# Kernel tuning notes

Measured on AMD Instinct MI355X. Metric: run time of the kernel, lower is better.

Reference implementation:

```python
import jax, jax.numpy as jnp
import numpy as np
import math

QUERY_DIM = 128
SCALE = 1.0 / math.sqrt(QUERY_DIM)

def setup_inputs() -> dict:
    key = jax.random.key(0)
    k1, k2, k3 = jax.random.split(key, 3)
    B, Q, K, D = 16, 2048, 2048, 128
    return {
        "query": jax.random.normal(k1, (B, Q, D), dtype=jnp.float32),
        "keys": jax.random.normal(k2, (B, K, D), dtype=jnp.float32),
        "values": jax.random.normal(k3, (B, K, D), dtype=jnp.float32),
    }

def reference(query, keys, values):
    # energy[b,q,k] = sum_d query[b,q,d] * keys[b,k,d], scaled then softmax over k
    energy = jnp.einsum("bqd,bkd->bqk", query, keys) * SCALE
    attn = jax.nn.softmax(energy, axis=2)
    # linear combination over values
    return jnp.einsum("bqk,bkv->bqv", attn, values)
```

## Files before the change

### kernel.cpp

```cpp
#include <hip/hip_runtime.h>
#include <hip/hip_bf16.h>


#define BATCH 16
#define QLEN 2048
#define KLEN 2048
#define DIM 128
#define BM 64
#define BN 64
#define NT (KLEN / BN)

#define KBYTES 16384
#define BUFBYTES 32768

typedef __attribute__((ext_vector_type(8))) short bf16x8;
typedef __attribute__((ext_vector_type(4))) float f32x4;

__device__ __forceinline__ short f2bf(float x) {
    union { float f; unsigned u; } v; v.f = x;
    unsigned r = v.u + 0x7FFFu + ((v.u >> 16) & 1u);
    return (short)(r >> 16);
}
__device__ __forceinline__ unsigned pkbf(float a, float b) {
    __hip_bfloat162 h = __float22bfloat162_rn(float2{a, b});
    union { __hip_bfloat162 h; unsigned u; } c; c.h = h;
    return c.u;
}

#define GLOAD_LDS16(g, l) \
    __builtin_amdgcn_global_load_lds((__attribute__((address_space(1))) void*)(g), \
                                     (__attribute__((address_space(3))) void*)(l), 16, 0, 0)

#define TSTR 72
__global__ __launch_bounds__(256) void prepass_kernel(
    const float* __restrict__ kg, const float* __restrict__ vg,
    unsigned short* __restrict__ Kws, unsigned short* __restrict__ Vtws)
{
    __shared__ unsigned short T[DIM * TSTR];
    const int tid = threadIdx.x;
    const int kb  = blockIdx.x * BN;
    const int b   = blockIdx.y;
    const float* kt = kg + ((size_t)b * KLEN + kb) * DIM;
    const float* vt = vg + ((size_t)b * KLEN + kb) * DIM;
    unsigned short* ko = Kws + ((size_t)b * KLEN + kb) * DIM;
#pragma unroll
    for (int j = 0; j < 8; ++j) {
        int idx = tid + 256 * j;
        int key = idx >> 5;
        int d4  = (idx & 31) * 4;
        float4 kv = *(const float4*)(kt + key * DIM + d4);
        uint2 w; w.x = pkbf(kv.x, kv.y); w.y = pkbf(kv.z, kv.w);
        *(uint2*)(ko + key * DIM + d4) = w;
        float4 vv = *(const float4*)(vt + key * DIM + d4);
        T[(d4 + 0) * TSTR + key] = (unsigned short)f2bf(vv.x);
        T[(d4 + 1) * TSTR + key] = (unsigned short)f2bf(vv.y);
        T[(d4 + 2) * TSTR + key] = (unsigned short)f2bf(vv.z);
        T[(d4 + 3) * TSTR + key] = (unsigned short)f2bf(vv.w);
    }
    __syncthreads();
    unsigned short* vo = Vtws + (size_t)b * DIM * KLEN + kb;
#pragma unroll
    for (int j = 0; j < 4; ++j) {
        int c = tid + 256 * j;
        int d = c >> 3;
        int g = c & 7;
        uint4 u = *(const uint4*)&T[d * TSTR + g * 8];
        *(uint4*)(vo + (size_t)d * KLEN + g * 8) = u;
    }
}

__global__ __launch_bounds__(256, 2) void attn_flash_kernel(
    const float* __restrict__ qg,
    const unsigned short* __restrict__ Kws,
    const unsigned short* __restrict__ Vtws,
    float* __restrict__ outg)
{
    __shared__ __align__(16) char SMC[2 * BUFBYTES];

    const int tid  = threadIdx.x;
    const int wave = tid >> 6;
    const int lane = tid & 63;
    const int lm   = lane & 15;
    const int quad = lane >> 4;
    const int rw   = wave >> 1;
    const int kw   = wave & 1;
    const int b     = blockIdx.y;
    const int qbase = blockIdx.x * BM + rw * 32;

    const float QSCALE = 0.08838834764831845f * 1.4426950408889634f;

    bf16x8 qfA[4], qfB[4];
    {
        const float* qrowA = qg + (size_t)(b * QLEN + qbase + lm) * DIM;
        const float* qrowB = qrowA + 16 * DIM;
#pragma unroll
        for (int dk = 0; dk < 4; ++dk) {
            int d0 = dk * 32 + quad * 8;
            float4 a = *(const float4*)(qrowA + d0);
            float4 c = *(const float4*)(qrowA + d0 + 4);
            uint4 u;
            u.x = pkbf(a.x*QSCALE, a.y*QSCALE); u.y = pkbf(a.z*QSCALE, a.w*QSCALE);
            u.z = pkbf(c.x*QSCALE, c.y*QSCALE); u.w = pkbf(c.z*QSCALE, c.w*QSCALE);
            qfA[dk] = *(bf16x8*)&u;
            float4 e = *(const float4*)(qrowB + d0);
            float4 g = *(const float4*)(qrowB + d0 + 4);
            uint4 v;
            v.x = pkbf(e.x*QSCALE, e.y*QSCALE); v.y = pkbf(e.z*QSCALE, e.w*QSCALE);
            v.z = pkbf(g.x*QSCALE, g.y*QSCALE); v.w = pkbf(g.z*QSCALE, g.w*QSCALE);
            qfB[dk] = *(bf16x8*)&v;
        }
    }

    f32x4 OA[8], OB[8];
#pragma unroll
    for (int i = 0; i < 8; ++i) { OA[i] = 0.0f; OB[i] = 0.0f; }
    float lrA = 0.f, lrB = 0.f;

    const unsigned short* Kb  = Kws  + (size_t)b * KLEN * DIM;
    const unsigned short* Vtb = Vtws + (size_t)b * DIM * KLEN;
    const char* kdma[4];
    const char* vdma[4];
    {
        int gk = lane & 15;
        int r0 = wave * 16 + (lane >> 4);
        int gv = lane & 7;
        int d0v = wave * 32 + (lane >> 3);
#pragma unroll
        for (int i = 0; i < 4; ++i) {
            int r = r0 + 4 * i;
            int key = (r & 3) | ((r & 4) << 1) | ((r & 8) << 1) | ((r & 16) >> 2) | (r & 32);
            kdma[i] = (const char*)Kb + key * 256 + ((gk ^ (r & 15)) << 4);
            int dv = d0v + 8 * i;
            vdma[i] = (const char*)Vtb + (size_t)dv * (KLEN * 2) + ((gv ^ (dv & 7)) << 4);
        }
    }

    int kfo[4];
#pragma unroll
    for (int dk = 0; dk < 4; ++dk)
        kfo[dk] = (kw * 32 + lm) * 256 + (((dk * 4 + quad) ^ lm) << 4);
    const int vfo = lm * 128 + (((kw * 4 + quad) ^ (lm & 7)) << 4);

    auto dma = [&](int tt, int bb) {
        char* ldsK = SMC + bb * BUFBYTES + wave * 4096;
        char* ldsV = ldsK + KBYTES;
        size_t ko = (size_t)tt * 16384;
        size_t vo = (size_t)tt * 128;
#pragma unroll
        for (int i = 0; i < 4; ++i) {
            GLOAD_LDS16(kdma[i] + ko, ldsK + i * 1024);
            GLOAD_LDS16(vdma[i] + vo, ldsV + i * 1024);
        }
    };

    dma(0, 0);
    __syncthreads();

    for (int t = 0; t < NT; ++t) {
        if (t + 1 < NT) dma(t + 1, (t + 1) & 1);

        const char* bufK = SMC + (t & 1) * BUFBYTES;
        const char* bufV = bufK + KBYTES;

        f32x4 S0a = 0.0f, S1a = 0.0f, S0b = 0.0f, S1b = 0.0f;
#pragma unroll
        for (int dk = 0; dk < 4; ++dk) {
            bf16x8 kf0 = *(const bf16x8*)(bufK + kfo[dk]);
            bf16x8 kf1 = *(const bf16x8*)(bufK + kfo[dk] + 4096);
            S0a = __builtin_amdgcn_mfma_f32_16x16x32_bf16(kf0, qfA[dk], S0a, 0, 0, 0);
            S0b = __builtin_amdgcn_mfma_f32_16x16x32_bf16(kf0, qfB[dk], S0b, 0, 0, 0);
            S1a = __builtin_amdgcn_mfma_f32_16x16x32_bf16(kf1, qfA[dk], S1a, 0, 0, 0);
            S1b = __builtin_amdgcn_mfma_f32_16x16x32_bf16(kf1, qfB[dk], S1b, 0, 0, 0);
        }

        float a0 = exp2f(S0a[0]), a1 = exp2f(S0a[1]), a2 = exp2f(S0a[2]), a3 = exp2f(S0a[3]);
        float a4 = exp2f(S1a[0]), a5 = exp2f(S1a[1]), a6 = exp2f(S1a[2]), a7 = exp2f(S1a[3]);
        float b0 = exp2f(S0b[0]), b1 = exp2f(S0b[1]), b2 = exp2f(S0b[2]), b3 = exp2f(S0b[3]);
        float b4 = exp2f(S1b[0]), b5 = exp2f(S1b[1]), b6 = exp2f(S1b[2]), b7 = exp2f(S1b[3]);
        uint4 puA, puB;
        puA.x = pkbf(a0,a1); puA.y = pkbf(a2,a3); puA.z = pkbf(a4,a5); puA.w = pkbf(a6,a7);
        puB.x = pkbf(b0,b1); puB.y = pkbf(b2,b3); puB.z = pkbf(b4,b5); puB.w = pkbf(b6,b7);
        bf16x8 pfA = *(bf16x8*)&puA;
        bf16x8 pfB = *(bf16x8*)&puB;
        lrA += ((a0+a1)+(a2+a3)) + ((a4+a5)+(a6+a7));
        lrB += ((b0+b1)+(b2+b3)) + ((b4+b5)+(b6+b7));

#pragma unroll
        for (int dt = 0; dt < 8; ++dt) {
            bf16x8 vf = *(const bf16x8*)(bufV + vfo + dt * 2048);
            OA[dt] = __builtin_amdgcn_mfma_f32_16x16x32_bf16(vf, pfA, OA[dt], 0, 0, 0);
            OB[dt] = __builtin_amdgcn_mfma_f32_16x16x32_bf16(vf, pfB, OB[dt], 0, 0, 0);
        }

        __syncthreads();
    }

    lrA += __shfl_xor(lrA, 16, 64); lrA += __shfl_xor(lrA, 32, 64);
    lrB += __shfl_xor(lrB, 16, 64); lrB += __shfl_xor(lrB, 32, 64);

    float* Orw = (float*)SMC + rw * 4288;
    if (kw == 1) {
#pragma unroll
        for (int dt = 0; dt < 8; ++dt) {
            *(f32x4*)&Orw[lm*132        + dt*16 + quad*4] = OA[dt];
            *(f32x4*)&Orw[(16+lm)*132   + dt*16 + quad*4] = OB[dt];
        }
        if (lane < 16)      Orw[4224 + lm]      = lrA;
        else if (lane < 32) Orw[4224 + 16 + lm] = lrB;
    }
    __syncthreads();
    if (kw == 0) {
        float invA = 1.0f / (lrA + Orw[4224 + lm]);
        float invB = 1.0f / (lrB + Orw[4224 + 16 + lm]);
        float* orowA = outg + (size_t)(b * QLEN + qbase + lm) * DIM;
        float* orowB = orowA + 16 * DIM;
#pragma unroll
        for (int dt = 0; dt < 8; ++dt) {
            f32x4 oA = *(const f32x4*)&Orw[lm*132      + dt*16 + quad*4];
            f32x4 oB = *(const f32x4*)&Orw[(16+lm)*132 + dt*16 + quad*4];
            *(f32x4*)&orowA[dt*16 + quad*4] = (OA[dt] + oA) * invA;
            *(f32x4*)&orowB[dt*16 + quad*4] = (OB[dt] + oB) * invB;
        }
    }
}

extern "C" void kernel_launch(void* const* d_in, const int* in_sizes, int n_in,
                              void* d_out, int out_size, void* d_ws, size_t ws_size,
                              hipStream_t stream) {
    const float* q = (const float*)d_in[0];
    const float* k = (const float*)d_in[1];
    const float* v = (const float*)d_in[2];
    float* o = (float*)d_out;
    unsigned short* Kws  = (unsigned short*)d_ws;
    unsigned short* Vtws = Kws + (size_t)BATCH * KLEN * DIM;
    dim3 grid(KLEN / BN, BATCH);
    prepass_kernel<<<grid, 256, 0, stream>>>(k, v, Kws, Vtws);
    dim3 grid2(QLEN / BM, BATCH);
    attn_flash_kernel<<<grid2, 256, 0, stream>>>(q, Kws, Vtws, o);
}
```

Measured before the change: 139.2 us.

## Split query rows across 8 waves, swizzle block order for XCD locality

Doubles the block to 512 threads so each wave handles 16 query rows instead of 32, halving accumulator registers and per-wave DMA to raise occupancy. Remaps block indices so consecutive blocks of the same batch land on the same XCD to improve L2 reuse of K/V. Replaces the bf16 pack intrinsic with manual rounding plus a byte-permute. Trades higher LDS fragment reads per MFMA for more resident waves.

```diff
diff --git a/kernel.cpp b/kernel.cpp
--- a/kernel.cpp
+++ b/kernel.cpp
@@ -22,9 +22,10 @@
     return (short)(r >> 16);
 }
 __device__ __forceinline__ unsigned pkbf(float a, float b) {
-    __hip_bfloat162 h = __float22bfloat162_rn(float2{a, b});
-    union { __hip_bfloat162 h; unsigned u; } c; c.h = h;
-    return c.u;
+    union { float f; unsigned u; } x, y; x.f = a; y.f = b;
+    unsigned ra = x.u + 0x7FFFu + ((x.u >> 16) & 1u);
+    unsigned rb = y.u + 0x7FFFu + ((y.u >> 16) & 1u);
+    return __builtin_amdgcn_perm(rb, ra, 0x07060302u);
 }
 
 #define GLOAD_LDS16(g, l) \
@@ -69,7 +70,7 @@
     }
 }
 
-__global__ __launch_bounds__(256, 2) void attn_flash_kernel(
+__global__ __launch_bounds__(512, 4) void attn_flash_kernel(
     const float* __restrict__ qg,
     const unsigned short* __restrict__ Kws,
     const unsigned short* __restrict__ Vtws,
@@ -84,49 +85,45 @@
     const int quad = lane >> 4;
     const int rw   = wave >> 1;
     const int kw   = wave & 1;
-    const int b     = blockIdx.y;
-    const int qbase = blockIdx.x * BM + rw * 32;
+
+    const int n  = blockIdx.y * gridDim.x + blockIdx.x;
+    const int np = (n & 7) * 64 + (n >> 3);
+    const int b     = np >> 5;
+    const int qbase = (np & 31) * BM + rw * 16;
 
     const float QSCALE = 0.08838834764831845f * 1.4426950408889634f;
 
-    bf16x8 qfA[4], qfB[4];
+    bf16x8 qf[4];
     {
-        const float* qrowA = qg + (size_t)(b * QLEN + qbase + lm) * DIM;
-        const float* qrowB = qrowA + 16 * DIM;
+        const float* qrow = qg + (size_t)(b * QLEN + qbase + lm) * DIM;
 #pragma unroll
         for (int dk = 0; dk < 4; ++dk) {
             int d0 = dk * 32 + quad * 8;
-            float4 a = *(const float4*)(qrowA + d0);
-            float4 c = *(const float4*)(qrowA + d0 + 4);
+            float4 a = *(const float4*)(qrow + d0);
+            float4 c = *(const float4*)(qrow + d0 + 4);
             uint4 u;
             u.x = pkbf(a.x*QSCALE, a.y*QSCALE); u.y = pkbf(a.z*QSCALE, a.w*QSCALE);
             u.z = pkbf(c.x*QSCALE, c.y*QSCALE); u.w = pkbf(c.z*QSCALE, c.w*QSCALE);
-            qfA[dk] = *(bf16x8*)&u;
-            float4 e = *(const float4*)(qrowB + d0);
-            float4 g = *(const float4*)(qrowB + d0 + 4);
-            uint4 v;
-            v.x = pkbf(e.x*QSCALE, e.y*QSCALE); v.y = pkbf(e.z*QSCALE, e.w*QSCALE);
-            v.z = pkbf(g.x*QSCALE, g.y*QSCALE); v.w = pkbf(g.z*QSCALE, g.w*QSCALE);
-            qfB[dk] = *(bf16x8*)&v;
-        }
-    }
-
-    f32x4 OA[8], OB[8];
-#pragma unroll
-    for (int i = 0; i < 8; ++i) { OA[i] = 0.0f; OB[i] = 0.0f; }
-    float lrA = 0.f, lrB = 0.f;
+            qf[dk] = *(bf16x8*)&u;
+        }
+    }
+
+    f32x4 O[8];
+#pragma unroll
+    for (int i = 0; i < 8; ++i) O[i] = 0.0f;
+    float lr = 0.f;
 
     const unsigned short* Kb  = Kws  + (size_t)b * KLEN * DIM;
     const unsigned short* Vtb = Vtws + (size_t)b * DIM * KLEN;
-    const char* kdma[4];
-    const char* vdma[4];
+    const char* kdma[2];
+    const char* vdma[2];
     {
-        int gk = lane & 15;
-        int r0 = wave * 16 + (lane >> 4);
-        int gv = lane & 7;
-        int d0v = wave * 32 + (lane >> 3);
-#pragma unroll
-        for (int i = 0; i < 4; ++i) {
+        int gk  = lane & 15;
+        int r0  = wave * 8 + (lane >> 4);
+        int gv  = lane & 7;
+        int d0v = wave * 16 + (lane >> 3);
+#pragma unroll
+        for (int i = 0; i < 2; ++i) {
             int r = r0 + 4 * i;
             int key = (r & 3) | ((r & 4) << 1) | ((r & 8) << 1) | ((r & 16) >> 2) | (r & 32);
             kdma[i] = (const char*)Kb + key * 256 + ((gk ^ (r & 15)) << 4);
@@ -142,12 +139,12 @@
     const int vfo = lm * 128 + (((kw * 4 + quad) ^ (lm & 7)) << 4);
 
     auto dma = [&](int tt, int bb) {
-        char* ldsK = SMC + bb * BUFBYTES + wave * 4096;
-        char* ldsV = ldsK + KBYTES;
+        char* ldsK = SMC + bb * BUFBYTES + wave * 2048;
+        char* ldsV = SMC + bb * BUFBYTES + KBYTES + wave * 2048;
         size_t ko = (size_t)tt * 16384;
         size_t vo = (size_t)tt * 128;
 #pragma unroll
-        for (int i = 0; i < 4; ++i) {
+        for (int i = 0; i < 2; ++i) {
             GLOAD_LDS16(kdma[i] + ko, ldsK + i * 1024);
             GLOAD_LDS16(vdma[i] + vo, ldsV + i * 1024);
         }
@@ -162,64 +159,49 @@
         const char* bufK = SMC + (t & 1) * BUFBYTES;
         const char* bufV = bufK + KBYTES;
 
-        f32x4 S0a = 0.0f, S1a = 0.0f, S0b = 0.0f, S1b = 0.0f;
+        f32x4 S0 = 0.0f, S1 = 0.0f;
 #pragma unroll
         for (int dk = 0; dk < 4; ++dk) {
             bf16x8 kf0 = *(const bf16x8*)(bufK + kfo[dk]);
             bf16x8 kf1 = *(const bf16x8*)(bufK + kfo[dk] + 4096);
-            S0a = __builtin_amdgcn_mfma_f32_16x16x32_bf16(kf0, qfA[dk], S0a, 0, 0, 0);
-            S0b = __builtin_amdgcn_mfma_f32_16x16x32_bf16(kf0, qfB[dk], S0b, 0, 0, 0);
-            S1a = __builtin_amdgcn_mfma_f32_16x16x32_bf16(kf1, qfA[dk], S1a, 0, 0, 0);
-            S1b = __builtin_amdgcn_mfma_f32_16x16x32_bf16(kf1, qfB[dk], S1b, 0, 0, 0);
-        }
-
-        float a0 = exp2f(S0a[0]), a1 = exp2f(S0a[1]), a2 = exp2f(S0a[2]), a3 = exp2f(S0a[3]);
-        float a4 = exp2f(S1a[0]), a5 = exp2f(S1a[1]), a6 = exp2f(S1a[2]), a7 = exp2f(S1a[3]);
-        float b0 = exp2f(S0b[0]), b1 = exp2f(S0b[1]), b2 = exp2f(S0b[2]), b3 = exp2f(S0b[3]);
-        float b4 = exp2f(S1b[0]), b5 = exp2f(S1b[1]), b6 = exp2f(S1b[2]), b7 = exp2f(S1b[3]);
-        uint4 puA, puB;
-        puA.x = pkbf(a0,a1); puA.y = pkbf(a2,a3); puA.z = pkbf(a4,a5); puA.w = pkbf(a6,a7);
-        puB.x = pkbf(b0,b1); puB.y = pkbf(b2,b3); puB.z = pkbf(b4,b5); puB.w = pkbf(b6,b7);
-        bf16x8 pfA = *(bf16x8*)&puA;
-        bf16x8 pfB = *(bf16x8*)&puB;
-        lrA += ((a0+a1)+(a2+a3)) + ((a4+a5)+(a6+a7));
-        lrB += ((b0+b1)+(b2+b3)) + ((b4+b5)+(b6+b7));
+            S0 = __builtin_amdgcn_mfma_f32_16x16x32_bf16(kf0, qf[dk], S0, 0, 0, 0);
+            S1 = __builtin_amdgcn_mfma_f32_16x16x32_bf16(kf1, qf[dk], S1, 0, 0, 0);
+        }
+
+        float a0 = exp2f(S0[0]), a1 = exp2f(S0[1]), a2 = exp2f(S0[2]), a3 = exp2f(S0[3]);
+        float a4 = exp2f(S1[0]), a5 = exp2f(S1[1]), a6 = exp2f(S1[2]), a7 = exp2f(S1[3]);
+        uint4 pu;
+        pu.x = pkbf(a0,a1); pu.y = pkbf(a2,a3); pu.z = pkbf(a4,a5); pu.w = pkbf(a6,a7);
+        bf16x8 pf = *(bf16x8*)&pu;
+        lr += ((a0+a1)+(a2+a3)) + ((a4+a5)+(a6+a7));
 
 #pragma unroll
         for (int dt = 0; dt < 8; ++dt) {
             bf16x8 vf = *(const bf16x8*)(bufV + vfo + dt * 2048);
-            OA[dt] = __builtin_amdgcn_mfma_f32_16x16x32_bf16(vf, pfA, OA[dt], 0, 0, 0);
-            OB[dt] = __builtin_amdgcn_mfma_f32_16x16x32_bf16(vf, pfB, OB[dt], 0, 0, 0);
+            O[dt] = __builtin_amdgcn_mfma_f32_16x16x32_bf16(vf, pf, O[dt], 0, 0, 0);
         }
 
         __syncthreads();
     }
 
-    lrA += __shfl_xor(lrA, 16, 64); lrA += __shfl_xor(lrA, 32, 64);
-    lrB += __shfl_xor(lrB, 16, 64); lrB += __shfl_xor(lrB, 32, 64);
-
-    float* Orw = (float*)SMC + rw * 4288;
+    lr += __shfl_xor(lr, 16, 64);
+    lr += __shfl_xor(lr, 32, 64);
+
+    float* Orw = (float*)SMC + rw * 2128;
     if (kw == 1) {
 #pragma unroll
-        for (int dt = 0; dt < 8; ++dt) {
-            *(f32x4*)&Orw[lm*132        + dt*16 + quad*4] = OA[dt];
-            *(f32x4*)&Orw[(16+lm)*132   + dt*16 + quad*4] = OB[dt];
-        }
-        if (lane < 16)      Orw[4224 + lm]      = lrA;
-        else if (lane < 32) Orw[4224 + 16 + lm] = lrB;
+        for (int dt = 0; dt < 8; ++dt)
+            *(f32x4*)&Orw[lm * 132 + dt * 16 + quad * 4] = O[dt];
+        if (lane < 16) Orw[2112 + lm] = lr;
     }
     __syncthreads();
     if (kw == 0) {
-        float invA = 1.0f / (lrA + Orw[4224 + lm]);
-        float invB = 1.0f / (lrB + Orw[4224 + 16 + lm]);
-        float* orowA = outg + (size_t)(b * QLEN + qbase + lm) * DIM;
-        float* orowB = orowA + 16 * DIM;
+        float inv = 1.0f / (lr + Orw[2112 + lm]);
+        float* orow = outg + (size_t)(b * QLEN + qbase + lm) * DIM;
 #pragma unroll
         for (int dt = 0; dt < 8; ++dt) {
-            f32x4 oA = *(const f32x4*)&Orw[lm*132      + dt*16 + quad*4];
-            f32x4 oB = *(const f32x4*)&Orw[(16+lm)*132 + dt*16 + quad*4];
-            *(f32x4*)&orowA[dt*16 + quad*4] = (OA[dt] + oA) * invA;
-            *(f32x4*)&orowB[dt*16 + quad*4] = (OB[dt] + oB) * invB;
+            f32x4 o = *(const f32x4*)&Orw[lm * 132 + dt * 16 + quad * 4];
+            *(f32x4*)&orow[dt * 16 + quad * 4] = (O[dt] + o) * inv;
         }
     }
 }
@@ -236,5 +218,5 @@
     dim3 grid(KLEN / BN, BATCH);
     prepass_kernel<<<grid, 256, 0, stream>>>(k, v, Kws, Vtws);
     dim3 grid2(QLEN / BM, BATCH);
-    attn_flash_kernel<<<grid2, 256, 0, stream>>>(q, Kws, Vtws, o);
-}
+    attn_flash_kernel<<<grid2, 512, 0, stream>>>(q, Kws, Vtws, o);
+}
```

Result: no change. 141.7 us (+1.7%).
